# Kernel tuning notes

Hardware: AMD Instinct MI355X
Metric: run time of the kernel (lower is better)

Reference implementation:

```python
import jax, jax.numpy as jnp
import numpy as np

TOKEN_BITS = 10
CODEBOOK_SIZE = 2 ** TOKEN_BITS  # 1024
COMMITMENT_COST = 0.25
ENTROPY_LOSS_WEIGHT = 0.1
ENTROPY_TEMPERATURE = 0.01
ENTROPY_GAMMA = 1.0
EPS = 1e-5


def _make_codebook():
    bits_to_indices = (2 ** jnp.arange(TOKEN_BITS)).astype(jnp.int32)          # [c]
    all_codes = jnp.arange(CODEBOOK_SIZE, dtype=jnp.int32)                      # [n]
    bits = ((all_codes[:, None] & bits_to_indices) != 0).astype(jnp.float32)    # [n, c]
    codebook = bits * 2.0 - 1.0                                                 # [n, c] in {-1,+1}
    return bits_to_indices, codebook


def setup_inputs() -> dict:
    key = jax.random.key(0)
    z = jax.random.normal(key, (16, TOKEN_BITS, 64, 64), dtype=jnp.float32)
    return {"z": z}


def reference(z):
    bits_to_indices, codebook = _make_codebook()

    # b c h w -> b h w c
    zp = jnp.transpose(z, (0, 2, 3, 1)).astype(jnp.float32)

    # sign quantization to {-1, +1}
    sign_mask = zp > 0.0
    z_q = jnp.where(sign_mask, 1.0, -1.0).astype(jnp.float32)

    # pack sign bits into codebook indices
    min_encoding_indices = jnp.sum(sign_mask.astype(jnp.int32) * bits_to_indices, axis=-1)  # [b,h,w]

    # commitment loss (stop-grad on the quantized target)
    commitment_loss = COMMITMENT_COST * jnp.mean((jax.lax.stop_gradient(z_q) - zp) ** 2)

    # entropy loss: logits = -d = 2 * z . codebook^T, softened by temperature
    logits = 2.0 * jnp.einsum('bhwc,nc->bhwn', zp, codebook)  # [b,h,w,n]
    log_probs = jax.nn.log_softmax(logits / ENTROPY_TEMPERATURE, axis=-1)
    probs = jnp.exp(log_probs)
    per_sample_entropy = jnp.mean(-jnp.sum(probs * log_probs, axis=-1))
    avg_probs = jnp.mean(probs, axis=(0, 1, 2))  # [n]
    avg_entropy = ENTROPY_GAMMA * (-jnp.sum(avg_probs * jnp.log(avg_probs + EPS)))
    entropy_loss = ENTROPY_LOSS_WEIGHT * (per_sample_entropy - avg_entropy)

    loss = commitment_loss + entropy_loss

    # straight-through estimator
    z_quantized = zp + jax.lax.stop_gradient(z_q - zp)
    # b h w c -> b c h w
    z_quantized = jnp.transpose(z_quantized, (0, 3, 1, 2))

    return z_quantized, loss, per_sample_entropy, min_encoding_indices
```

## Files before the change

### kernel.cpp

```cpp
#include <hip/hip_runtime.h>

#define NCH    10
#define NCODE  1024
#define NLOC   65536
#define NZ     655360
#define GRID   256
#define THR    256
#define NHIST  8
#define NPART  (GRID * 4)

__device__ __forceinline__ float wave_reduce_sum(float v) {
#pragma unroll
    for (int off = 32; off > 0; off >>= 1)
        v += __shfl_down(v, off, 64);
    return v;
}

__global__ __launch_bounds__(THR) void lfq_main(
    const float* __restrict__ z, float* __restrict__ out,
    float* __restrict__ wsH, float* __restrict__ wsC, float* __restrict__ wsE)
{
    __shared__ float sR[NCH][THR];
    __shared__ unsigned short sM[NCH][THR];

    const int tid  = threadIdx.x;
    const int loc  = blockIdx.x * THR + tid;
    const int b    = loc >> 12;
    const int base = b * (NCH * 4096) + (loc & 4095);
    float* hist = wsH + (blockIdx.x & (NHIST - 1)) * NCODE;

    float zc[NCH];
#pragma unroll
    for (int c = 0; c < NCH; ++c) zc[c] = z[base + c * 4096];

    float commit = 0.f, ent = 0.f, pstar = 1.f;
    int idx = 0, k = 0;
#pragma unroll
    for (int c = 0; c < NCH; ++c) {
        float zv = zc[c];
        bool bit = zv > 0.f;
        float s = bit ? 1.f : -1.f;
        __builtin_nontemporal_store(s, out + base + c * 4096);
        if (bit) idx |= (1 << c);
        float d = s - zv;
        commit += d * d;
        float a = fabsf(zv) * 400.f;
        if (a < 23.0f) {
            float e = __expf(-a);
            float inv = 1.f / (1.f + e);
            ent += __logf(1.f + e) + a * e * inv;
            pstar *= inv;
            sR[k][tid] = e;
            sM[k][tid] = (unsigned short)(1u << c);
            ++k;
        }
    }
    __builtin_nontemporal_store((float)idx, out + NZ + 2 + loc);

    atomicAdd(&hist[idx], pstar);
    for (int m = 1; m < (1 << k); ++m) {
        float w = pstar;
        int code = idx;
        for (int j = 0; j < k; ++j)
            if (m & (1 << j)) { w *= sR[j][tid]; code ^= sM[j][tid]; }
        atomicAdd(&hist[code], w);
    }

    float cw = wave_reduce_sum(commit);
    float ew = wave_reduce_sum(ent);
    const int wave = tid >> 6, lane = tid & 63;
    if (lane == 0) {
        wsC[blockIdx.x * 4 + wave] = cw;
        wsE[blockIdx.x * 4 + wave] = ew;
    }
}

__global__ __launch_bounds__(1024) void lfq_final(
    const float* __restrict__ wsH, const float* __restrict__ wsC,
    const float* __restrict__ wsE, float* __restrict__ out)
{
    const int n = threadIdx.x;
    float s = 0.f;
#pragma unroll
    for (int h = 0; h < NHIST; ++h) s += wsH[h * NCODE + n];
    float avg_p = s * (1.f / (float)NLOC);
    float term = -avg_p * __logf(avg_p + 1e-5f);
    float c = wsC[n];
    float e = wsE[n];
    float tw = wave_reduce_sum(term);
    float cw = wave_reduce_sum(c);
    float ew = wave_reduce_sum(e);
    __shared__ float red[48];
    const int wave = n >> 6, lane = n & 63;
    if (lane == 0) { red[wave] = tw; red[16 + wave] = cw; red[32 + wave] = ew; }
    __syncthreads();
    if (n == 0) {
        float avg_ent = 0.f, cs = 0.f, es = 0.f;
#pragma unroll
        for (int w = 0; w < 16; ++w) {
            avg_ent += red[w]; cs += red[16 + w]; es += red[32 + w];
        }
        float commitment = 0.25f * cs * (1.f / (float)NZ);
        float per_sample = es * (1.f / (float)NLOC);
        out[NZ]     = commitment + 0.1f * (per_sample - avg_ent);
        out[NZ + 1] = per_sample;
    }
}

extern "C" void kernel_launch(void* const* d_in, const int* in_sizes, int n_in,
                              void* d_out, int out_size, void* d_ws, size_t ws_size,
                              hipStream_t stream) {
    const float* z = (const float*)d_in[0];
    float* out = (float*)d_out;
    float* wsH = (float*)d_ws;
    float* wsC = wsH + NHIST * NCODE;
    float* wsE = wsC + NPART;

    lfq_main<<<GRID, THR, 0, stream>>>(z, out, wsH, wsC, wsE);
    lfq_final<<<1, 1024, 0, stream>>>(wsH, wsC, wsE, out);
}
```

Before: 72.85 us.

## Split channels across half-waves and quadruple grid for more parallelism

Each location is now handled by two lanes, each processing five channels, with the partial index, probability and near-zero count combined via cross-lane shuffles. The grid grows to 1024 blocks of 128 threads (64 locations per block) to spread the memory-bound load and store stream across more CUs. Input loads become nontemporal. The histogram scatter loop still runs only on half the lanes, so that part sees more divergence, and the final kernel now reads two partial sums per thread.

```diff
diff --git a/kernel.cpp b/kernel.cpp
--- a/kernel.cpp
+++ b/kernel.cpp
@@ -4,10 +4,11 @@
 #define NCODE  1024
 #define NLOC   65536
 #define NZ     655360
-#define GRID   256
-#define THR    256
+#define GRID   1024
+#define THR    128
+#define LPB    64
 #define NHIST  8
-#define NPART  (GRID * 4)
+#define NPART  (GRID * 2)
 
 __device__ __forceinline__ float wave_reduce_sum(float v) {
 #pragma unroll
@@ -20,28 +21,35 @@
     const float* __restrict__ z, float* __restrict__ out,
     float* __restrict__ wsH, float* __restrict__ wsC, float* __restrict__ wsE)
 {
-    __shared__ float sR[NCH][THR];
-    __shared__ unsigned short sM[NCH][THR];
+    __shared__ float sR[LPB][NCH];
+    __shared__ unsigned short sM[LPB][NCH];
 
     const int tid  = threadIdx.x;
-    const int loc  = blockIdx.x * THR + tid;
+    const int wv   = tid >> 6;
+    const int lane = tid & 63;
+    const int sub  = lane >> 5;
+    const int l32  = lane & 31;
+    const int lloc = wv * 32 + l32;
+    const int loc  = blockIdx.x * LPB + lloc;
     const int b    = loc >> 12;
     const int base = b * (NCH * 4096) + (loc & 4095);
+    const int c0   = sub * 5;
     float* hist = wsH + (blockIdx.x & (NHIST - 1)) * NCODE;
 
-    float zc[NCH];
+    float zc[5];
 #pragma unroll
-    for (int c = 0; c < NCH; ++c) zc[c] = z[base + c * 4096];
+    for (int i = 0; i < 5; ++i)
+        zc[i] = __builtin_nontemporal_load(z + base + (c0 + i) * 4096);
 
     float commit = 0.f, ent = 0.f, pstar = 1.f;
     int idx = 0, k = 0;
 #pragma unroll
-    for (int c = 0; c < NCH; ++c) {
-        float zv = zc[c];
+    for (int i = 0; i < 5; ++i) {
+        float zv = zc[i];
         bool bit = zv > 0.f;
         float s = bit ? 1.f : -1.f;
-        __builtin_nontemporal_store(s, out + base + c * 4096);
-        if (bit) idx |= (1 << c);
+        __builtin_nontemporal_store(s, out + base + (c0 + i) * 4096);
+        if (bit) idx |= (1 << (c0 + i));
         float d = s - zv;
         commit += d * d;
         float a = fabsf(zv) * 400.f;
@@ -50,28 +58,41 @@
             float inv = 1.f / (1.f + e);
             ent += __logf(1.f + e) + a * e * inv;
             pstar *= inv;
-            sR[k][tid] = e;
-            sM[k][tid] = (unsigned short)(1u << c);
+            sR[lloc][c0 + k] = e;
+            sM[lloc][c0 + k] = (unsigned short)(1u << (c0 + i));
             ++k;
         }
     }
-    __builtin_nontemporal_store((float)idx, out + NZ + 2 + loc);
 
-    atomicAdd(&hist[idx], pstar);
-    for (int m = 1; m < (1 << k); ++m) {
-        float w = pstar;
-        int code = idx;
-        for (int j = 0; j < k; ++j)
-            if (m & (1 << j)) { w *= sR[j][tid]; code ^= sM[j][tid]; }
-        atomicAdd(&hist[code], w);
+    const int   idx_o = __shfl_xor(idx, 32, 64);
+    const float p_o   = __shfl_xor(pstar, 32, 64);
+    const int   k_o   = __shfl_xor(k, 32, 64);
+
+    if (sub == 0) {
+        const int idxT = idx | idx_o;
+        const float pT = pstar * p_o;
+        __builtin_nontemporal_store((float)idxT, out + NZ + 2 + loc);
+
+        atomicAdd(&hist[idxT], pT);
+        const int k0 = k, kt = k + k_o;
+        for (int m = 1; m < (1 << kt); ++m) {
+            float w = pT;
+            int code = idxT;
+            for (int j = 0; j < kt; ++j)
+                if (m & (1 << j)) {
+                    const int slot = (j < k0) ? j : (5 + j - k0);
+                    w *= sR[lloc][slot];
+                    code ^= sM[lloc][slot];
+                }
+            atomicAdd(&hist[code], w);
+        }
     }
 
     float cw = wave_reduce_sum(commit);
     float ew = wave_reduce_sum(ent);
-    const int wave = tid >> 6, lane = tid & 63;
     if (lane == 0) {
-        wsC[blockIdx.x * 4 + wave] = cw;
-        wsE[blockIdx.x * 4 + wave] = ew;
+        wsC[blockIdx.x * 2 + wv] = cw;
+        wsE[blockIdx.x * 2 + wv] = ew;
     }
 }
 
@@ -85,8 +106,8 @@
     for (int h = 0; h < NHIST; ++h) s += wsH[h * NCODE + n];
     float avg_p = s * (1.f / (float)NLOC);
     float term = -avg_p * __logf(avg_p + 1e-5f);
-    float c = wsC[n];
-    float e = wsE[n];
+    float c = wsC[n] + wsC[1024 + n];
+    float e = wsE[n] + wsE[1024 + n];
     float tw = wave_reduce_sum(term);
     float cw = wave_reduce_sum(c);
     float ew = wave_reduce_sum(e);
```

Result: no change. 72.02 us (-1.1%).
